# Kernel tuning notes

Hardware: AMD Instinct MI355X
Metric: run time of the kernel (lower is better)

Reference implementation:

```python
import jax, jax.numpy as jnp
import numpy as np

N_NODES = 100000
N_EDGES = 1600000
IN_CH = 128
HID = 128
OUT_CH = 40


def setup_inputs() -> dict:
    key = jax.random.key(0)
    ks = jax.random.split(key, 8)
    x = jax.random.normal(ks[0], (N_NODES, IN_CH), dtype=jnp.float32)
    edge_index = jax.random.randint(ks[1], (2, N_EDGES), 0, N_NODES, dtype=jnp.int64)
    s1 = 1.0 / np.sqrt(IN_CH)
    s2 = 1.0 / np.sqrt(HID)
    # SAGEConv layer 1: lin_l (applied to aggregated neighbors, has bias), lin_r (applied to root, no bias)
    Wl1 = jax.random.uniform(ks[2], (IN_CH, HID), jnp.float32, -s1, s1)
    b1 = jnp.zeros((HID,), jnp.float32)
    Wr1 = jax.random.uniform(ks[3], (IN_CH, HID), jnp.float32, -s1, s1)
    # SAGEConv layer 2
    Wl2 = jax.random.uniform(ks[4], (HID, OUT_CH), jnp.float32, -s2, s2)
    b2 = jnp.zeros((OUT_CH,), jnp.float32)
    Wr2 = jax.random.uniform(ks[5], (HID, OUT_CH), jnp.float32, -s2, s2)
    return {"x": x, "edge_index": edge_index, "Wl1": Wl1, "b1": b1, "Wr1": Wr1,
            "Wl2": Wl2, "b2": b2, "Wr2": Wr2}


def _sage_conv(x, src, dst, Wl, b, Wr):
    # mean-aggregate source-node features onto target nodes (PyG SAGEConv, aggr='mean')
    msg_sum = jax.ops.segment_sum(x[src], dst, num_segments=N_NODES)  # [N, F]
    deg = jax.ops.segment_sum(jnp.ones((src.shape[0],), x.dtype), dst, num_segments=N_NODES)
    aggr = msg_sum / jnp.maximum(deg, 1.0)[:, None]
    return aggr @ Wl + b + x @ Wr


def reference(x, edge_index, Wl1, b1, Wr1, Wl2, b2, Wr2):
    src, dst = edge_index[0], edge_index[1]
    h = _sage_conv(x, src, dst, Wl1, b1, Wr1)
    h = jax.nn.relu(h)  # dropout is identity in eval mode
    h = _sage_conv(h, src, dst, Wl2, b2, Wr2)
    return jax.nn.log_softmax(h, axis=-1)
```

## Files before the change

### kernel.cpp

```cpp
#include <hip/hip_runtime.h>
#include <math.h>

#define NN 100000
#define NE 1600000
#define NBUK ((NN + 255) / 256)
#define CAP 5120
#define NBLK_A 500
#define EPB (NE / NBLK_A)
#define GPB (EPB / 4)
#define MT ((NN + 127) / 128)
#define MPAD ((size_t)MT * 128)
#define PACK_B 192
#define CVT_B0 (NBLK_A + PACK_B)
#define FRONT_GRID 2048

typedef __attribute__((ext_vector_type(8))) short short8;
typedef __attribute__((ext_vector_type(4))) float f32x4;
typedef __attribute__((ext_vector_type(4))) int i32x4;
typedef unsigned short ushort_t;
typedef unsigned int uint_t;

__device__ inline ushort_t f2bf(float f) {
    uint_t u = __builtin_bit_cast(uint_t, f);
    u += 0x7FFFu + ((u >> 16) & 1u);
    return (ushort_t)(u >> 16);
}
__device__ inline float bits2f(uint_t u) { return __builtin_bit_cast(float, u); }
__device__ inline float lo16(uint_t u) { return bits2f(u << 16); }
__device__ inline float hi16(uint_t u) { return bits2f(u & 0xFFFF0000u); }

__device__ inline void gload_lds16(const void* g, void* l) {
    __builtin_amdgcn_global_load_lds(
        (const __attribute__((address_space(1))) unsigned int*)g,
        (__attribute__((address_space(3))) unsigned int*)l, 16, 0, 0);
}

__global__ __launch_bounds__(256) void front(const float* __restrict__ x,
                                             ushort_t* __restrict__ xb,
                                             const float* __restrict__ Wl1,
                                             const float* __restrict__ Wr1,
                                             const float* __restrict__ Wl2,
                                             const float* __restrict__ Wr2,
                                             ushort_t* __restrict__ W1T,
                                             ushort_t* __restrict__ W2T,
                                             const int* __restrict__ ei,
                                             int* __restrict__ bhist,
                                             int* __restrict__ bhp) {
    __shared__ int h[NBUK];
    int bid = blockIdx.x, tid = threadIdx.x;
    if (bid < NBLK_A) {
        for (int i = tid; i < NBUK; i += 256) h[i] = 0;
        __syncthreads();
        const i32x4* dsts = (const i32x4*)(ei + NE + bid * EPB);
        for (int g = tid; g < GPB; g += 256) {
            i32x4 d = __builtin_nontemporal_load(dsts + g);
#pragma unroll
            for (int j = 0; j < 4; ++j) atomicAdd(&h[d[j] >> 8], 1);
        }
        __syncthreads();
        for (int i = tid; i < NBUK; i += 256) {
            int c = h[i];
            bhp[bid * NBUK + i] = c;
            if (c) atomicAdd(&bhist[i], c);
        }
    } else if (bid < CVT_B0) {
        int gid = (bid - NBLK_A) * 256 + tid;
        if (gid < 256 * 128) {
            int n = gid >> 7, k = gid & 127;
            float v = (n < 128) ? Wl1[k * 128 + n] : Wr1[k * 128 + (n - 128)];
            W1T[gid] = f2bf(v);
        } else {
            int g = gid - 256 * 128;
            if (g < 128 * 128) {
                int n = g >> 7, k = g & 127;
                float v = 0.0f;
                if (n < 40)      v = Wl2[k * 40 + n];
                else if (n < 80) v = Wr2[k * 40 + (n - 40)];
                W2T[g] = f2bf(v);
            }
        }
    } else {
        const int total = NN * 128 / 8;
        const int nb = FRONT_GRID - CVT_B0;
        const f32x4* src = (const f32x4*)x;
        for (int g = (bid - CVT_B0) * 256 + tid; g < total; g += nb * 256) {
            f32x4 v0 = __builtin_nontemporal_load(src + (size_t)g * 2);
            f32x4 v1 = __builtin_nontemporal_load(src + (size_t)g * 2 + 1);
            i32x4 o;
            o[0] = ((uint_t)f2bf(v0[1]) << 16) | (uint_t)f2bf(v0[0]);
            o[1] = ((uint_t)f2bf(v0[3]) << 16) | (uint_t)f2bf(v0[2]);
            o[2] = ((uint_t)f2bf(v1[1]) << 16) | (uint_t)f2bf(v1[0]);
            o[3] = ((uint_t)f2bf(v1[3]) << 16) | (uint_t)f2bf(v1[2]);
            *(i32x4*)(xb + (size_t)g * 8) = o;
        }
    }
}

__global__ __launch_bounds__(512) void scan_buckets(const int* __restrict__ bhist,
                                                    int* __restrict__ boff,
                                                    int* __restrict__ gcur,
                                                    int* __restrict__ offsets) {
    __shared__ int part[512];
    int t = threadIdx.x;
    int v = (t < NBUK) ? bhist[t] : 0;
    part[t] = v;
    __syncthreads();
    for (int d = 1; d < 512; d <<= 1) {
        int tmp = (t >= d) ? part[t - d] : 0;
        __syncthreads();
        part[t] += tmp;
        __syncthreads();
    }
    if (t <= NBUK) {
        int excl = (t == 0) ? 0 : part[t - 1];
        boff[t] = excl;
        if (t < NBUK) gcur[t] = excl;
    }
    if (t == 0) offsets[NN] = NE;
}

__global__ __launch_bounds__(256) void bin_pass(const int* __restrict__ ei,
                                                const int* __restrict__ bhp,
                                                int* __restrict__ gcur,
                                                int* __restrict__ pairs) {
    __shared__ int h[NBUK];
    __shared__ int base[NBUK];
    int bid = blockIdx.x, tid = threadIdx.x;
    const int* myh = bhp + bid * NBUK;
    for (int i = tid; i < NBUK; i += 256) {
        int c = myh[i];
        base[i] = c ? atomicAdd(&gcur[i], c) : 0;
        h[i] = 0;
    }
    __syncthreads();
    int e0 = bid * EPB;
    const i32x4* dsts = (const i32x4*)(ei + NE + e0);
    const i32x4* srcs = (const i32x4*)(ei + e0);
    for (int g = tid; g < GPB; g += 256) {
        i32x4 d = __builtin_nontemporal_load(dsts + g);
        i32x4 s = __builtin_nontemporal_load(srcs + g);
#pragma unroll
        for (int j = 0; j < 4; ++j) {
            int buk = d[j] >> 8;
            int pos = base[buk] + atomicAdd(&h[buk], 1);
            pairs[pos] = (s[j] << 8) | (d[j] & 255);
        }
    }
}

__global__ __launch_bounds__(256) void sort_buckets(const int* __restrict__ boff,
                                                    const int* __restrict__ pairs,
                                                    int* __restrict__ offsets,
                                                    int* __restrict__ ssrc) {
    __shared__ int plds[CAP];
    __shared__ int slds[CAP];
    __shared__ int cnt[256];
    __shared__ int excl[256];
    int buk = blockIdx.x, tid = threadIdx.x;
    int bstart = boff[buk], bend = boff[buk + 1];
    int count = min(bend - bstart, CAP);
    int lo = buk << 8;
    cnt[tid] = 0;
    __syncthreads();
    for (int j = tid; j < count; j += 256) {
        int p = pairs[bstart + j];
        plds[j] = p;
        atomicAdd(&cnt[p & 255], 1);
    }
    __syncthreads();
    int c = cnt[tid];
    excl[tid] = c;
    __syncthreads();
    for (int d = 1; d < 256; d <<= 1) {
        int tmp = (tid >= d) ? excl[tid - d] : 0;
        __syncthreads();
        excl[tid] += tmp;
        __syncthreads();
    }
    int myExcl = excl[tid] - c;
    __syncthreads();
    excl[tid] = myExcl;
    cnt[tid] = 0;
    __syncthreads();
    for (int j = tid; j < count; j += 256) {
        int p = plds[j];
        int loc = p & 255;
        int pos = excl[loc] + atomicAdd(&cnt[loc], 1);
        slds[pos] = p >> 8;
    }
    __syncthreads();
    for (int j = tid; j < count; j += 256) ssrc[bstart + j] = slds[j];
    if (lo + tid < NN) offsets[lo + tid] = bstart + myExcl;
}

__global__ __launch_bounds__(256, 2) void gemm_mfma(const ushort_t* __restrict__ A,
                                                    const ushort_t* __restrict__ Bt,
                                                    ushort_t* __restrict__ G,
                                                    ushort_t* __restrict__ Croot,
                                                    int M, int split, int rootEnd, int gstride) {
    __shared__ __align__(16) char As[128 * 256];
    __shared__ __align__(16) char Bs[128 * 256];
    int tid = threadIdx.x;
    int lane = tid & 63, wid = tid >> 6;
    int quad = lane >> 4, l15 = lane & 15;
    int wm = (wid & 1) * 64, wn = (wid >> 1) * 64;
    int mBase = blockIdx.x * 128, nBase = blockIdx.y * 128;
    int rootW = rootEnd - split;

    const char* aT = (const char*)(A + (size_t)mBase * 128);
    const char* bT = (const char*)(Bt + (size_t)nBase * 128);
#pragma unroll
    for (int ii = 0; ii < 8; ++ii) {
        int rr = (wid * 8 + ii) * 4 + quad;
        int src = rr * 256 + ((l15 * 16) ^ ((rr & 7) << 4));
        int ldsb = (wid * 8 + ii) * 1024;
        gload_lds16(aT + src, As + ldsb);
        gload_lds16(bT + src, Bs + ldsb);
    }
    asm volatile("s_waitcnt vmcnt(0)" ::: "memory");
    __syncthreads();

    f32x4 acc[4][4];
#pragma unroll
    for (int i = 0; i < 4; ++i)
#pragma unroll
        for (int j = 0; j < 4; ++j) acc[i][j] = (f32x4){0.f, 0.f, 0.f, 0.f};

#pragma unroll
    for (int kk = 0; kk < 4; ++kk) {
        int kByte = kk * 64 + quad * 16;
        short8 af[4], bfr[4];
#pragma unroll
        for (int i = 0; i < 4; ++i) {
            int row = wm + i * 16 + l15;
            af[i] = *(const short8*)(As + row * 256 + (kByte ^ ((row & 7) << 4)));
        }
#pragma unroll
        for (int j = 0; j < 4; ++j) {
            int row = wn + j * 16 + l15;
            bfr[j] = *(const short8*)(Bs + row * 256 + (kByte ^ ((row & 7) << 4)));
        }
#pragma unroll
        for (int i = 0; i < 4; ++i)
#pragma unroll
            for (int j = 0; j < 4; ++j)
                acc[i][j] = __builtin_amdgcn_mfma_f32_16x16x32_bf16(af[i], bfr[j],
                                                                    acc[i][j], 0, 0, 0);
    }

#pragma unroll
    for (int i = 0; i < 4; ++i) {
#pragma unroll
        for (int r = 0; r < 4; ++r) {
            int m = mBase + wm + i * 16 + quad * 4 + r;
            if (m >= M) continue;
#pragma unroll
            for (int j = 0; j < 4; ++j) {
                int n = nBase + wn + j * 16 + l15;
                float v = acc[i][j][r];
                if (n < split) G[(size_t)m * gstride + n] = f2bf(v);
                else if (n < rootEnd) Croot[(size_t)m * rootW + (n - split)] = f2bf(v);
            }
        }
    }
}

__global__ __launch_bounds__(256) void aggregate1(const int* __restrict__ offsets,
                                                  const int* __restrict__ ssrc,
                                                  const ushort_t* __restrict__ G1,
                                                  const ushort_t* __restrict__ C1root,
                                                  const float* __restrict__ b1,
                                                  ushort_t* __restrict__ s1b) {
    int w = (blockIdx.x * blockDim.x + threadIdx.x) >> 6;
    int lane = threadIdx.x & 63;
    if (w >= NN) return;
    int start = offsets[w], end = offsets[w + 1];
    int g = lane >> 4, q = lane & 15;
    const char* Gb = (const char*)G1;
    int qb = q << 4;
    float a0 = 0.f, a1 = 0.f, a2 = 0.f, a3 = 0.f, a4 = 0.f, a5 = 0.f, a6 = 0.f, a7 = 0.f;
    for (int base = start; base < end; base += 64) {
        int cnt = min(64, end - base);
        int idx = (base + lane < end) ? ssrc[base + lane] : 0;
        int j = 0;
        for (; j + 16 <= cnt; j += 16) {
            int s0 = __shfl(idx, j + g, 64);
            int s1 = __shfl(idx, j + 4 + g, 64);
            int s2 = __shfl(idx, j + 8 + g, 64);
            int s3 = __shfl(idx, j + 12 + g, 64);
            uint4 u0 = *(const uint4*)(Gb + (s0 << 8) + qb);
            uint4 u1 = *(const uint4*)(Gb + (s1 << 8) + qb);
            uint4 u2 = *(const uint4*)(Gb + (s2 << 8) + qb);
            uint4 u3 = *(const uint4*)(Gb + (s3 << 8) + qb);
            a0 += (lo16(u0.x) + lo16(u1.x)) + (lo16(u2.x) + lo16(u3.x));
            a1 += (hi16(u0.x) + hi16(u1.x)) + (hi16(u2.x) + hi16(u3.x));
            a2 += (lo16(u0.y) + lo16(u1.y)) + (lo16(u2.y) + lo16(u3.y));
            a3 += (hi16(u0.y) + hi16(u1.y)) + (hi16(u2.y) + hi16(u3.y));
            a4 += (lo16(u0.z) + lo16(u1.z)) + (lo16(u2.z) + lo16(u3.z));
            a5 += (hi16(u0.z) + hi16(u1.z)) + (hi16(u2.z) + hi16(u3.z));
            a6 += (lo16(u0.w) + lo16(u1.w)) + (lo16(u2.w) + lo16(u3.w));
            a7 += (hi16(u0.w) + hi16(u1.w)) + (hi16(u2.w) + hi16(u3.w));
        }
        for (; j + 8 <= cnt; j += 8) {
            int s0 = __shfl(idx, j + g, 64);
            int s1 = __shfl(idx, j + 4 + g, 64);
            uint4 u0 = *(const uint4*)(Gb + (s0 << 8) + qb);
            uint4 u1 = *(const uint4*)(Gb + (s1 << 8) + qb);
            a0 += lo16(u0.x) + lo16(u1.x);
            a1 += hi16(u0.x) + hi16(u1.x);
            a2 += lo16(u0.y) + lo16(u1.y);
            a3 += hi16(u0.y) + hi16(u1.y);
            a4 += lo16(u0.z) + lo16(u1.z);
            a5 += hi16(u0.z) + hi16(u1.z);
            a6 += lo16(u0.w) + lo16(u1.w);
            a7 += hi16(u0.w) + hi16(u1.w);
        }
        for (; j < cnt; j += 4) {
            int e = j + g;
            int s0 = __shfl(idx, (e < cnt) ? e : 0, 64);
            if (e < cnt) {
                uint4 u0 = *(const uint4*)(Gb + (s0 << 8) + qb);
                a0 += lo16(u0.x); a1 += hi16(u0.x);
                a2 += lo16(u0.y); a3 += hi16(u0.y);
                a4 += lo16(u0.z); a5 += hi16(u0.z);
                a6 += lo16(u0.w); a7 += hi16(u0.w);
            }
        }
    }
    a0 += __shfl_xor(a0, 16, 64); a0 += __shfl_xor(a0, 32, 64);
    a1 += __shfl_xor(a1, 16, 64); a1 += __shfl_xor(a1, 32, 64);
    a2 += __shfl_xor(a2, 16, 64); a2 += __shfl_xor(a2, 32, 64);
    a3 += __shfl_xor(a3, 16, 64); a3 += __shfl_xor(a3, 32, 64);
    a4 += __shfl_xor(a4, 16, 64); a4 += __shfl_xor(a4, 32, 64);
    a5 += __shfl_xor(a5, 16, 64); a5 += __shfl_xor(a5, 32, 64);
    a6 += __shfl_xor(a6, 16, 64); a6 += __shfl_xor(a6, 32, 64);
    a7 += __shfl_xor(a7, 16, 64); a7 += __shfl_xor(a7, 32, 64);
    if (g == 0) {
        float inv = 1.0f / fmaxf((float)(end - start), 1.0f);
        uint4 rv = *(const uint4*)((const char*)C1root + (size_t)w * 256 + qb);
        float4 c0 = *(const float4*)(b1 + q * 8);
        float4 c1 = *(const float4*)(b1 + q * 8 + 4);
        float h0 = fmaxf(a0 * inv + c0.x + lo16(rv.x), 0.f);
        float h1 = fmaxf(a1 * inv + c0.y + hi16(rv.x), 0.f);
        float h2 = fmaxf(a2 * inv + c0.z + lo16(rv.y), 0.f);
        float h3 = fmaxf(a3 * inv + c0.w + hi16(rv.y), 0.f);
        float h4 = fmaxf(a4 * inv + c1.x + lo16(rv.z), 0.f);
        float h5 = fmaxf(a5 * inv + c1.y + hi16(rv.z), 0.f);
        float h6 = fmaxf(a6 * inv + c1.z + lo16(rv.w), 0.f);
        float h7 = fmaxf(a7 * inv + c1.w + hi16(rv.w), 0.f);
        uint4 o;
        o.x = ((uint_t)f2bf(h1) << 16) | (uint_t)f2bf(h0);
        o.y = ((uint_t)f2bf(h3) << 16) | (uint_t)f2bf(h2);
        o.z = ((uint_t)f2bf(h5) << 16) | (uint_t)f2bf(h4);
        o.w = ((uint_t)f2bf(h7) << 16) | (uint_t)f2bf(h6);
        *(uint4*)((char*)s1b + (size_t)w * 256 + qb) = o;
    }
}

__global__ __launch_bounds__(256) void aggregate2(const int* __restrict__ offsets,
                                                  const int* __restrict__ ssrc,
                                                  const ushort_t* __restrict__ G2,
                                                  const ushort_t* __restrict__ C2root,
                                                  const float* __restrict__ b2,
                                                  float* __restrict__ out) {
    int w = (blockIdx.x * blockDim.x + threadIdx.x) >> 6;
    int lane = threadIdx.x & 63;
    if (w >= NN) return;
    int start = offsets[w], end = offsets[w + 1];
    int g = lane >> 4, q = lane & 15;
    bool act = q < 10;
    int qb = q << 3;
    const char* Gb = (const char*)G2;
    float a0 = 0.f, a1 = 0.f, a2 = 0.f, a3 = 0.f;
    for (int base = start; base < end; base += 64) {
        int cnt = min(64, end - base);
        int idx = (base + lane < end) ? ssrc[base + lane] : 0;
        int j = 0;
        for (; j + 16 <= cnt; j += 16) {
            int s0 = __shfl(idx, j + g, 64);
            int s1 = __shfl(idx, j + 4 + g, 64);
            int s2 = __shfl(idx, j + 8 + g, 64);
            int s3 = __shfl(idx, j + 12 + g, 64);
            if (act) {
                uint2 u0 = *(const uint2*)(Gb + (s0 << 7) + qb);
                uint2 u1 = *(const uint2*)(Gb + (s1 << 7) + qb);
                uint2 u2 = *(const uint2*)(Gb + (s2 << 7) + qb);
                uint2 u3 = *(const uint2*)(Gb + (s3 << 7) + qb);
                a0 += (lo16(u0.x) + lo16(u1.x)) + (lo16(u2.x) + lo16(u3.x));
                a1 += (hi16(u0.x) + hi16(u1.x)) + (hi16(u2.x) + hi16(u3.x));
                a2 += (lo16(u0.y) + lo16(u1.y)) + (lo16(u2.y) + lo16(u3.y));
                a3 += (hi16(u0.y) + hi16(u1.y)) + (hi16(u2.y) + hi16(u3.y));
            }
        }
        for (; j + 8 <= cnt; j += 8) {
            int s0 = __shfl(idx, j + g, 64);
            int s1 = __shfl(idx, j + 4 + g, 64);
            if (act) {
                uint2 u0 = *(const uint2*)(Gb + (s0 << 7) + qb);
                uint2 u1 = *(const uint2*)(Gb + (s1 << 7) + qb);
                a0 += lo16(u0.x) + lo16(u1.x);
                a1 += hi16(u0.x) + hi16(u1.x);
                a2 += lo16(u0.y) + lo16(u1.y);
                a3 += hi16(u0.y) + hi16(u1.y);
            }
        }
        for (; j < cnt; j += 4) {
            int e = j + g;
            int s0 = __shfl(idx, (e < cnt) ? e : 0, 64);
            if (act && e < cnt) {
                uint2 u0 = *(const uint2*)(Gb + (s0 << 7) + qb);
                a0 += lo16(u0.x); a1 += hi16(u0.x);
                a2 += lo16(u0.y); a3 += hi16(u0.y);
            }
        }
    }
    a0 += __shfl_xor(a0, 16, 64); a0 += __shfl_xor(a0, 32, 64);
    a1 += __shfl_xor(a1, 16, 64); a1 += __shfl_xor(a1, 32, 64);
    a2 += __shfl_xor(a2, 16, 64); a2 += __shfl_xor(a2, 32, 64);
    a3 += __shfl_xor(a3, 16, 64); a3 += __shfl_xor(a3, 32, 64);
    if (g == 0) {
        float inv = 1.0f / fmaxf((float)(end - start), 1.0f);
        float v0 = -INFINITY, v1 = -INFINITY, v2 = -INFINITY, v3 = -INFINITY;
        if (act) {
            uint2 rv = *(const uint2*)((const char*)C2root + (size_t)w * 80 + qb);
            float4 bb = *(const float4*)(b2 + q * 4);
            v0 = a0 * inv + bb.x + lo16(rv.x);
            v1 = a1 * inv + bb.y + hi16(rv.x);
            v2 = a2 * inv + bb.z + lo16(rv.y);
            v3 = a3 * inv + bb.w + hi16(rv.y);
        }
        float m = fmaxf(fmaxf(v0, v1), fmaxf(v2, v3));
#pragma unroll
        for (int d = 8; d >= 1; d >>= 1) m = fmaxf(m, __shfl_xor(m, d, 64));
        float e = act ? (expf(v0 - m) + expf(v1 - m)) + (expf(v2 - m) + expf(v3 - m)) : 0.f;
#pragma unroll
        for (int d = 8; d >= 1; d >>= 1) e += __shfl_xor(e, d, 64);
        float lse = m + logf(e);
        if (act) {
            float4 o = make_float4(v0 - lse, v1 - lse, v2 - lse, v3 - lse);
            *(float4*)(out + (size_t)w * 40 + q * 4) = o;
        }
    }
}

extern "C" void kernel_launch(void* const* d_in, const int* in_sizes, int n_in,
                              void* d_out, int out_size, void* d_ws, size_t ws_size,
                              hipStream_t stream) {
    const float* x   = (const float*)d_in[0];
    const int*   ei  = (const int*)d_in[1];
    const float* Wl1 = (const float*)d_in[2];
    const float* b1  = (const float*)d_in[3];
    const float* Wr1 = (const float*)d_in[4];
    const float* Wl2 = (const float*)d_in[5];
    const float* b2  = (const float*)d_in[6];
    const float* Wr2 = (const float*)d_in[7];
    float* out = (float*)d_out;

    char* ws = (char*)d_ws;
    size_t off = 0;
    auto alloc = [&](size_t bytes) -> void* {
        void* p = ws + off;
        off = (off + bytes + 255) & ~(size_t)255;
        return p;
    };
    int*      bhist   = (int*)alloc((size_t)NBUK * 4);
    int*      boff    = (int*)alloc((size_t)(NBUK + 1) * 4);
    int*      gcur    = (int*)alloc((size_t)NBUK * 4);
    int*      bhp     = (int*)alloc((size_t)NBLK_A * NBUK * 4);
    int*      pairs   = (int*)alloc((size_t)NE * 4);
    int*      offsets = (int*)alloc((size_t)(NN + 1) * 4);
    int*      ssrc    = (int*)alloc((size_t)NE * 4);
    ushort_t* W1T     = (ushort_t*)alloc((size_t)256 * 128 * 2);
    ushort_t* W2T     = (ushort_t*)alloc((size_t)128 * 128 * 2);
    ushort_t* xb      = (ushort_t*)alloc(MPAD * 128 * 2);
    ushort_t* G1      = (ushort_t*)alloc((size_t)NN * 128 * 2);
    ushort_t* C1root  = (ushort_t*)alloc((size_t)NN * 128 * 2);
    ushort_t* s1b     = (ushort_t*)alloc(MPAD * 128 * 2);
    ushort_t* G2      = (ushort_t*)alloc((size_t)NN * 64 * 2);
    ushort_t* C2root  = (ushort_t*)alloc((size_t)NN * 40 * 2);

    hipMemsetAsync(bhist, 0, (size_t)NBUK * 4, stream);

    front<<<FRONT_GRID, 256, 0, stream>>>(x, xb, Wl1, Wr1, Wl2, Wr2, W1T, W2T, ei, bhist, bhp);
    scan_buckets<<<1, 512, 0, stream>>>(bhist, boff, gcur, offsets);
    bin_pass<<<NBLK_A, 256, 0, stream>>>(ei, bhp, gcur, pairs);
    sort_buckets<<<NBUK, 256, 0, stream>>>(boff, pairs, offsets, ssrc);

    dim3 g1(MT, 2);
    gemm_mfma<<<g1, 256, 0, stream>>>(xb, W1T, G1, C1root, NN, 128, 256, 128);

    aggregate1<<<(NN * 64 + 255) / 256, 256, 0, stream>>>(offsets, ssrc, G1, C1root, b1, s1b);

    dim3 g2(MT, 1);
    gemm_mfma<<<g2, 256, 0, stream>>>(s1b, W2T, G2, C2root, NN, 40, 80, 64);

    aggregate2<<<(NN * 64 + 255) / 256, 256, 0, stream>>>(offsets, ssrc, G2, C2root, b2, out);
}
```

Before: 335.3 us.

## Fuse bucket sort with layer-1 GEMM, drop global histogram atomics, compact G2

```diff
diff --git a/kernel.cpp b/kernel.cpp
--- a/kernel.cpp
+++ b/kernel.cpp
@@ -44,7 +44,6 @@
                                              ushort_t* __restrict__ W1T,
                                              ushort_t* __restrict__ W2T,
                                              const int* __restrict__ ei,
-                                             int* __restrict__ bhist,
                                              int* __restrict__ bhp) {
     __shared__ int h[NBUK];
     int bid = blockIdx.x, tid = threadIdx.x;
@@ -58,11 +57,7 @@
             for (int j = 0; j < 4; ++j) atomicAdd(&h[d[j] >> 8], 1);
         }
         __syncthreads();
-        for (int i = tid; i < NBUK; i += 256) {
-            int c = h[i];
-            bhp[bid * NBUK + i] = c;
-            if (c) atomicAdd(&bhist[i], c);
-        }
+        for (int i = tid; i < NBUK; i += 256) bhp[bid * NBUK + i] = h[i];
     } else if (bid < CVT_B0) {
         int gid = (bid - NBLK_A) * 256 + tid;
         if (gid < 256 * 128) {
@@ -96,13 +91,16 @@
     }
 }
 
-__global__ __launch_bounds__(512) void scan_buckets(const int* __restrict__ bhist,
+__global__ __launch_bounds__(512) void scan_buckets(const int* __restrict__ bhp,
                                                     int* __restrict__ boff,
                                                     int* __restrict__ gcur,
                                                     int* __restrict__ offsets) {
     __shared__ int part[512];
     int t = threadIdx.x;
-    int v = (t < NBUK) ? bhist[t] : 0;
+    int v = 0;
+    if (t < NBUK) {
+        for (int b = 0; b < NBLK_A; ++b) v += bhp[b * NBUK + t];
+    }
     part[t] = v;
     __syncthreads();
     for (int d = 1; d < 512; d <<= 1) {
@@ -148,64 +146,18 @@
     }
 }
 
-__global__ __launch_bounds__(256) void sort_buckets(const int* __restrict__ boff,
-                                                    const int* __restrict__ pairs,
-                                                    int* __restrict__ offsets,
-                                                    int* __restrict__ ssrc) {
-    __shared__ int plds[CAP];
-    __shared__ int slds[CAP];
-    __shared__ int cnt[256];
-    __shared__ int excl[256];
-    int buk = blockIdx.x, tid = threadIdx.x;
-    int bstart = boff[buk], bend = boff[buk + 1];
-    int count = min(bend - bstart, CAP);
-    int lo = buk << 8;
-    cnt[tid] = 0;
-    __syncthreads();
-    for (int j = tid; j < count; j += 256) {
-        int p = pairs[bstart + j];
-        plds[j] = p;
-        atomicAdd(&cnt[p & 255], 1);
-    }
-    __syncthreads();
-    int c = cnt[tid];
-    excl[tid] = c;
-    __syncthreads();
-    for (int d = 1; d < 256; d <<= 1) {
-        int tmp = (tid >= d) ? excl[tid - d] : 0;
-        __syncthreads();
-        excl[tid] += tmp;
-        __syncthreads();
-    }
-    int myExcl = excl[tid] - c;
-    __syncthreads();
-    excl[tid] = myExcl;
-    cnt[tid] = 0;
-    __syncthreads();
-    for (int j = tid; j < count; j += 256) {
-        int p = plds[j];
-        int loc = p & 255;
-        int pos = excl[loc] + atomicAdd(&cnt[loc], 1);
-        slds[pos] = p >> 8;
-    }
-    __syncthreads();
-    for (int j = tid; j < count; j += 256) ssrc[bstart + j] = slds[j];
-    if (lo + tid < NN) offsets[lo + tid] = bstart + myExcl;
-}
-
-__global__ __launch_bounds__(256, 2) void gemm_mfma(const ushort_t* __restrict__ A,
-                                                    const ushort_t* __restrict__ Bt,
-                                                    ushort_t* __restrict__ G,
-                                                    ushort_t* __restrict__ Croot,
-                                                    int M, int split, int rootEnd, int gstride) {
-    __shared__ __align__(16) char As[128 * 256];
-    __shared__ __align__(16) char Bs[128 * 256];
-    int tid = threadIdx.x;
+template <int LAYER>
+__device__ inline void gemm_tile(char* As, char* Bs,
+                                 const ushort_t* __restrict__ A,
+                                 const ushort_t* __restrict__ Bt,
+                                 ushort_t* __restrict__ O0,
+                                 ushort_t* __restrict__ O1,
+                                 ushort_t* __restrict__ Croot,
+                                 int bx, int by, int tid, int M) {
     int lane = tid & 63, wid = tid >> 6;
     int quad = lane >> 4, l15 = lane & 15;
     int wm = (wid & 1) * 64, wn = (wid >> 1) * 64;
-    int mBase = blockIdx.x * 128, nBase = blockIdx.y * 128;
-    int rootW = rootEnd - split;
+    int mBase = bx * 128, nBase = by * 128;
 
     const char* aT = (const char*)(A + (size_t)mBase * 128);
     const char* bT = (const char*)(Bt + (size_t)nBase * 128);
@@ -258,11 +210,83 @@
             for (int j = 0; j < 4; ++j) {
                 int n = nBase + wn + j * 16 + l15;
                 float v = acc[i][j][r];
-                if (n < split) G[(size_t)m * gstride + n] = f2bf(v);
-                else if (n < rootEnd) Croot[(size_t)m * rootW + (n - split)] = f2bf(v);
+                if (LAYER == 1) {
+                    if (n < 128) O0[(size_t)m * 128 + n] = f2bf(v);
+                    else if (n < 256) Croot[(size_t)m * 128 + (n - 128)] = f2bf(v);
+                } else {
+                    if (n < 32) O0[(size_t)m * 32 + n] = f2bf(v);
+                    else if (n < 40) O1[(size_t)m * 8 + (n - 32)] = f2bf(v);
+                    else if (n < 80) Croot[(size_t)m * 40 + (n - 40)] = f2bf(v);
+                }
             }
         }
     }
+}
+
+__global__ __launch_bounds__(256, 2) void sort_gemm1(const int* __restrict__ boff,
+                                                     const int* __restrict__ pairs,
+                                                     int* __restrict__ offsets,
+                                                     int* __restrict__ ssrc,
+                                                     const ushort_t* __restrict__ A,
+                                                     const ushort_t* __restrict__ Bt,
+                                                     ushort_t* __restrict__ G,
+                                                     ushort_t* __restrict__ Croot) {
+    __shared__ __align__(16) char smem[65536];
+    int bid = blockIdx.x, tid = threadIdx.x;
+    if (bid < NBUK) {
+        int* plds = (int*)smem;
+        int* slds = (int*)(smem + CAP * 4);
+        int* cnt  = (int*)(smem + CAP * 8);
+        int* excl = cnt + 256;
+        int buk = bid;
+        int bstart = boff[buk], bend = boff[buk + 1];
+        int count = min(bend - bstart, CAP);
+        int lo = buk << 8;
+        cnt[tid] = 0;
+        __syncthreads();
+        for (int j = tid; j < count; j += 256) {
+            int p = pairs[bstart + j];
+            plds[j] = p;
+            atomicAdd(&cnt[p & 255], 1);
+        }
+        __syncthreads();
+        int c = cnt[tid];
+        excl[tid] = c;
+        __syncthreads();
+        for (int d = 1; d < 256; d <<= 1) {
+            int tmp = (tid >= d) ? excl[tid - d] : 0;
+            __syncthreads();
+            excl[tid] += tmp;
+            __syncthreads();
+        }
+        int myExcl = excl[tid] - c;
+        __syncthreads();
+        excl[tid] = myExcl;
+        cnt[tid] = 0;
+        __syncthreads();
+        for (int j = tid; j < count; j += 256) {
+            int p = plds[j];
+            int loc = p & 255;
+            int pos = excl[loc] + atomicAdd(&cnt[loc], 1);
+            slds[pos] = p >> 8;
+        }
+        __syncthreads();
+        for (int j = tid; j < count; j += 256) ssrc[bstart + j] = slds[j];
+        if (lo + tid < NN) offsets[lo + tid] = bstart + myExcl;
+    } else {
+        int gb = bid - NBUK;
+        int bx = gb % MT, by = gb / MT;
+        gemm_tile<1>(smem, smem + 32768, A, Bt, G, (ushort_t*)nullptr, Croot, bx, by, tid, NN);
+    }
+}
+
+__global__ __launch_bounds__(256, 2) void gemm2_k(const ushort_t* __restrict__ A,
+                                                  const ushort_t* __restrict__ Bt,
+                                                  ushort_t* __restrict__ G2a,
+                                                  ushort_t* __restrict__ G2b,
+                                                  ushort_t* __restrict__ C2root) {
+    __shared__ __align__(16) char smem[65536];
+    gemm_tile<2>(smem, smem + 32768, A, Bt, G2a, G2b, C2root, blockIdx.x, 0, threadIdx.x, NN);
 }
 
 __global__ __launch_bounds__(256) void aggregate1(const int* __restrict__ offsets,
@@ -359,7 +383,8 @@
 
 __global__ __launch_bounds__(256) void aggregate2(const int* __restrict__ offsets,
                                                   const int* __restrict__ ssrc,
-                                                  const ushort_t* __restrict__ G2,
+                                                  const ushort_t* __restrict__ G2a,
+                                                  const ushort_t* __restrict__ G2b,
                                                   const ushort_t* __restrict__ C2root,
                                                   const float* __restrict__ b2,
                                                   float* __restrict__ out) {
@@ -369,8 +394,10 @@
     int start = offsets[w], end = offsets[w + 1];
     int g = lane >> 4, q = lane & 15;
     bool act = q < 10;
-    int qb = q << 3;
-    const char* Gb = (const char*)G2;
+    const char* tbl;
+    int rsh, off0;
+    if (q < 8) { tbl = (const char*)G2a; rsh = 6; off0 = q * 8; }
+    else       { tbl = (const char*)G2b; rsh = 4; off0 = (q - 8) * 8; }
     float a0 = 0.f, a1 = 0.f, a2 = 0.f, a3 = 0.f;
     for (int base = start; base < end; base += 64) {
         int cnt = min(64, end - base);
@@ -382,10 +409,10 @@
             int s2 = __shfl(idx, j + 8 + g, 64);
             int s3 = __shfl(idx, j + 12 + g, 64);
             if (act) {
-                uint2 u0 = *(const uint2*)(Gb + (s0 << 7) + qb);
-                uint2 u1 = *(const uint2*)(Gb + (s1 << 7) + qb);
-                uint2 u2 = *(const uint2*)(Gb + (s2 << 7) + qb);
-                uint2 u3 = *(const uint2*)(Gb + (s3 << 7) + qb);
+                uint2 u0 = *(const uint2*)(tbl + ((size_t)s0 << rsh) + off0);
+                uint2 u1 = *(const uint2*)(tbl + ((size_t)s1 << rsh) + off0);
+                uint2 u2 = *(const uint2*)(tbl + ((size_t)s2 << rsh) + off0);
+                uint2 u3 = *(const uint2*)(tbl + ((size_t)s3 << rsh) + off0);
                 a0 += (lo16(u0.x) + lo16(u1.x)) + (lo16(u2.x) + lo16(u3.x));
                 a1 += (hi16(u0.x) + hi16(u1.x)) + (hi16(u2.x) + hi16(u3.x));
                 a2 += (lo16(u0.y) + lo16(u1.y)) + (lo16(u2.y) + lo16(u3.y));
@@ -396,8 +423,8 @@
             int s0 = __shfl(idx, j + g, 64);
             int s1 = __shfl(idx, j + 4 + g, 64);
             if (act) {
-                uint2 u0 = *(const uint2*)(Gb + (s0 << 7) + qb);
-                uint2 u1 = *(const uint2*)(Gb + (s1 << 7) + qb);
+                uint2 u0 = *(const uint2*)(tbl + ((size_t)s0 << rsh) + off0);
+                uint2 u1 = *(const uint2*)(tbl + ((size_t)s1 << rsh) + off0);
                 a0 += lo16(u0.x) + lo16(u1.x);
                 a1 += hi16(u0.x) + hi16(u1.x);
                 a2 += lo16(u0.y) + lo16(u1.y);
@@ -408,7 +435,7 @@
             int e = j + g;
             int s0 = __shfl(idx, (e < cnt) ? e : 0, 64);
             if (act && e < cnt) {
-                uint2 u0 = *(const uint2*)(Gb + (s0 << 7) + qb);
+                uint2 u0 = *(const uint2*)(tbl + ((size_t)s0 << rsh) + off0);
                 a0 += lo16(u0.x); a1 += hi16(u0.x);
                 a2 += lo16(u0.y); a3 += hi16(u0.y);
             }
@@ -422,7 +449,7 @@
         float inv = 1.0f / fmaxf((float)(end - start), 1.0f);
         float v0 = -INFINITY, v1 = -INFINITY, v2 = -INFINITY, v3 = -INFINITY;
         if (act) {
-            uint2 rv = *(const uint2*)((const char*)C2root + (size_t)w * 80 + qb);
+            uint2 rv = *(const uint2*)((const char*)C2root + (size_t)w * 80 + (q << 3));
             float4 bb = *(const float4*)(b2 + q * 4);
             v0 = a0 * inv + bb.x + lo16(rv.x);
             v1 = a1 * inv + bb.y + hi16(rv.x);
@@ -463,7 +490,6 @@
         off = (off + bytes + 255) & ~(size_t)255;
         return p;
     };
-    int*      bhist   = (int*)alloc((size_t)NBUK * 4);
     int*      boff    = (int*)alloc((size_t)(NBUK + 1) * 4);
     int*      gcur    = (int*)alloc((size_t)NBUK * 4);
     int*      bhp     = (int*)alloc((size_t)NBLK_A * NBUK * 4);
@@ -476,23 +502,17 @@
     ushort_t* G1      = (ushort_t*)alloc((size_t)NN * 128 * 2);
     ushort_t* C1root  = (ushort_t*)alloc((size_t)NN * 128 * 2);
     ushort_t* s1b     = (ushort_t*)alloc(MPAD * 128 * 2);
-    ushort_t* G2      = (ushort_t*)alloc((size_t)NN * 64 * 2);
+    ushort_t* G2a     = (ushort_t*)alloc((size_t)NN * 32 * 2);
+    ushort_t* G2b     = (ushort_t*)alloc((size_t)NN * 8 * 2);
     ushort_t* C2root  = (ushort_t*)alloc((size_t)NN * 40 * 2);
 
-    hipMemsetAsync(bhist, 0, (size_t)NBUK * 4, stream);
-
-    front<<<FRONT_GRID, 256, 0, stream>>>(x, xb, Wl1, Wr1, Wl2, Wr2, W1T, W2T, ei, bhist, bhp);
-    scan_buckets<<<1, 512, 0, stream>>>(bhist, boff, gcur, offsets);
+    front<<<FRONT_GRID, 256, 0, stream>>>(x, xb, Wl1, Wr1, Wl2, Wr2, W1T, W2T, ei, bhp);
+    scan_buckets<<<1, 512, 0, stream>>>(bhp, boff, gcur, offsets);
     bin_pass<<<NBLK_A, 256, 0, stream>>>(ei, bhp, gcur, pairs);
-    sort_buckets<<<NBUK, 256, 0, stream>>>(boff, pairs, offsets, ssrc);
-
-    dim3 g1(MT, 2);
-    gemm_mfma<<<g1, 256, 0, stream>>>(xb, W1T, G1, C1root, NN, 128, 256, 128);
-
+    sort_gemm1<<<NBUK + MT * 2, 256, 0, stream>>>(boff, pairs, offsets, ssrc,
+                                                  xb, W1T, G1, C1root);
     aggregate1<<<(NN * 64 + 255) / 256, 256, 0, stream>>>(offsets, ssrc, G1, C1root, b1, s1b);
-
-    dim3 g2(MT, 1);
-    gemm_mfma<<<g2, 256, 0, stream>>>(s1b, W2T, G2, C2root, NN, 40, 80, 64);
-
-    aggregate2<<<(NN * 64 + 255) / 256, 256, 0, stream>>>(offsets, ssrc, G2, C2root, b2, out);
-}
+    gemm2_k<<<MT, 256, 0, stream>>>(s1b, W2T, G2a, G2b, C2root);
+    aggregate2<<<(NN * 64 + 255) / 256, 256, 0, stream>>>(offsets, ssrc, G2a, G2b,
+                                                          C2root, b2, out);
+}
```

Measured after the change: 326.8 us. 1.03x faster.
